# Optimization experiments

Measured on AMD Instinct MI355X. Metric: run time of the kernel, lower is better.

Reference implementation:

```python
import jax, jax.numpy as jnp
import numpy as np
from jax import lax


def _conv(x, w, b, padding):
    # x: NCHW, w: OIHW
    y = lax.conv_general_dilated(x, w, (1, 1), padding,
                                 dimension_numbers=('NCHW', 'OIHW', 'NCHW'))
    return y + b[None, :, None, None]


def setup_inputs() -> dict:
    key = jax.random.key(0)
    ks = jax.random.split(key, 24)
    B = 64
    d = {
        'p2': jax.random.normal(ks[0], (B, 128, 64, 128), jnp.float32),
        'p3': jax.random.normal(ks[1], (B, 128, 32, 64), jnp.float32),
        'p4': jax.random.normal(ks[2], (B, 128, 16, 32), jnp.float32),
        'p5': jax.random.normal(ks[3], (B, 512, 8, 16), jnp.float32),
    }
    def w(k, shape, fan_in):
        return jax.random.normal(k, shape, jnp.float32) * (1.0 / np.sqrt(fan_in))
    # smooth convs 3x3, 128->128
    for i, name in enumerate(['s1', 's2', 's3']):
        d['w_' + name] = w(ks[4 + 2 * i], (128, 128, 3, 3), 128 * 9)
        d['b_' + name] = jnp.zeros((128,), jnp.float32)
    # tidy convs 1x1
    tidy_cin = [128, 128, 128, 512]
    for i in range(4):
        d['w_t%d' % (i + 1)] = w(ks[10 + i], (1, tidy_cin[i], 1, 1), tidy_cin[i])
        d['b_t%d' % (i + 1)] = jnp.zeros((1,), jnp.float32)
    # pl convs (kH,1) on single channel
    pl_kh = [64, 32, 16, 8]
    for i in range(4):
        d['w_pl%d' % (i + 1)] = w(ks[14 + i], (1, 1, pl_kh[i], 1), pl_kh[i])
        d['b_pl%d' % (i + 1)] = jnp.zeros((1,), jnp.float32)
    return d


def reference(p2, p3, p4, p5,
              w_s1, b_s1, w_s2, b_s2, w_s3, b_s3,
              w_t1, b_t1, w_t2, b_t2, w_t3, b_t3, w_t4, b_t4,
              w_pl1, b_pl1, w_pl2, b_pl2, w_pl3, b_pl3, w_pl4, b_pl4):
    B = p2.shape[0]
    # smooth + relu (p5 has no smooth in the original module)
    q2 = jax.nn.relu(_conv(p2, w_s1, b_s1, 'SAME'))
    q3 = jax.nn.relu(_conv(p3, w_s2, b_s2, 'SAME'))
    q4 = jax.nn.relu(_conv(p4, w_s3, b_s3, 'SAME'))
    # tidy 1x1 -> single score channel
    t1 = _conv(q2, w_t1, b_t1, 'VALID')
    t2 = _conv(q3, w_t2, b_t2, 'VALID')
    t3 = _conv(q4, w_t3, b_t3, 'VALID')
    t4 = _conv(p5, w_t4, b_t4, 'VALID')
    # column-pooling convs collapse height to 1 -> per-column scores
    c1 = _conv(t1, w_pl1, b_pl1, 'VALID').reshape(B, -1)  # [B,128]
    c2 = _conv(t2, w_pl2, b_pl2, 'VALID').reshape(B, -1)  # [B,64]
    c3 = _conv(t3, w_pl3, b_pl3, 'VALID').reshape(B, -1)  # [B,32]
    c4 = _conv(t4, w_pl4, b_pl4, 'VALID').reshape(B, -1)  # [B,16]
    return jnp.concatenate([c1, c2, c3, c4], axis=1)      # [B,240]
```

## Files before the change

kernel.cpp:

```cpp
#include <hip/hip_runtime.h>


typedef short s8v __attribute__((ext_vector_type(8)));
typedef float f4v __attribute__((ext_vector_type(4)));

__device__ __forceinline__ unsigned short f32_bf16_rne(float f) {
  union { float f; unsigned int u; } v;
  v.f = f;
  unsigned int u = v.u;
  u += 0x7FFFu + ((u >> 16) & 1u);
  return (unsigned short)(u >> 16);
}

__device__ __forceinline__ void gld_lds16(const unsigned short* g, unsigned short* l) {
  __builtin_amdgcn_global_load_lds(
      (const __attribute__((address_space(1))) unsigned int*)g,
      (__attribute__((address_space(3))) unsigned int*)l, 16, 0, 0);
}

__global__ void prep_x_k(const float* __restrict__ p,
                         unsigned short* __restrict__ out,
                         int H, int W) {
  size_t idx = (size_t)blockIdx.x * 256 + threadIdx.x;
  int HW = H * W;
  int w = (int)(idx % W);
  size_t r = idx / W;
  int h = (int)(r % H); r /= H;
  int qg = (int)(r & 3); r >>= 2;
  int chunk = (int)(r & 3); r >>= 2;
  int b = (int)r;
  const float* src = p + (((size_t)(b * 128 + chunk * 32 + qg * 8)) * H + h) * W + w;
  s8v v;
#pragma unroll
  for (int i = 0; i < 8; ++i) v[i] = (short)f32_bf16_rne(src[(size_t)i * HW]);
  *(s8v*)(out + idx * 8) = v;
}

__global__ void prep_w_k(const float* __restrict__ w1,
                         const float* __restrict__ w2,
                         const float* __restrict__ w3,
                         unsigned short* __restrict__ out) {
  int idx = blockIdx.x * 256 + threadIdx.x;
  if (idx >= 442368) return;
  int i    = idx & 7;
  int cout = (idx >> 3) & 127;
  int t    = idx >> 10;
  int qg = t & 3; t >>= 2;
  int kw = t % 3; t /= 3;
  int kh = t % 3; t /= 3;
  int chunk = t & 3; t >>= 2;
  int s = t;
  const float* w = (s == 0) ? w1 : ((s == 1) ? w2 : w3);
  int cin = chunk * 32 + qg * 8 + i;
  out[idx] = f32_bf16_rne(w[((cout * 128 + cin) * 3 + kh) * 3 + kw]);
}

__global__ void init_out_k(float* __restrict__ out,
                           const float* bt1, const float* bt2,
                           const float* bt3, const float* bt4,
                           const float* wpl1, const float* bpl1,
                           const float* wpl2, const float* bpl2,
                           const float* wpl3, const float* bpl3,
                           const float* wpl4, const float* bpl4) {
  int idx = blockIdx.x * 256 + threadIdx.x;
  if (idx >= 64 * 240) return;
  int c = idx % 240;
  const float* wpl; const float* bpl; const float* bt; int H;
  if (c < 128)      { wpl = wpl1; bpl = bpl1; bt = bt1; H = 64; }
  else if (c < 192) { wpl = wpl2; bpl = bpl2; bt = bt2; H = 32; }
  else if (c < 224) { wpl = wpl3; bpl = bpl3; bt = bt3; H = 16; }
  else              { wpl = wpl4; bpl = bpl4; bt = bt4; H = 8;  }
  float s = 0.f;
  for (int h = 0; h < H; ++h) s += wpl[h];
  out[idx] = bt[0] * s + bpl[0];
}

__global__ void level4_k(const float* __restrict__ p5,
                         const float* __restrict__ w_t4,
                         const float* __restrict__ w_pl4,
                         float* __restrict__ out) {
  int b = blockIdx.x;
  int z = blockIdx.y;
  int t = threadIdx.x;
  int w = t & 15, g = t >> 4;
  const float* base = p5 + (size_t)b * 65536 + z * 16384;
  const float* wt = w_t4 + z * 128;
  float acc = 0.f;
  for (int j = g; j < 1024; j += 16) {
    acc += wt[j >> 3] * w_pl4[j & 7] * base[j * 16 + w];
  }
  acc += __shfl_xor(acc, 16);
  acc += __shfl_xor(acc, 32);
  if ((t & 48) == 0) atomicAdd(&out[b * 240 + 224 + w], acc);
}

template<int H, int W, int R, int COLBASE>
__global__ __launch_bounds__(256, 2)
void conv_level_k(const unsigned short* __restrict__ xp,
                  const unsigned short* __restrict__ wl,
                  const float* __restrict__ b_s,
                  const float* __restrict__ w_t,
                  const float* __restrict__ w_pl,
                  float* __restrict__ out) {
  constexpr int ROWS = R + 2;
  constexpr int WP = W + 2;
  __shared__ __align__(16) unsigned short Xs[4][ROWS][WP][8];
  __shared__ __align__(16) unsigned short Ws[3][4][128][8];

  const int tid = threadIdx.x;
  const int wave = tid >> 6, lane = tid & 63;
  const int lm = lane & 15, q = lane >> 4;
  const int h0 = blockIdx.x * R;
  const int b  = blockIdx.y;

  int rr[4], ww[4], xbase[4];
#pragma unroll
  for (int nt = 0; nt < 4; ++nt) {
    int n = wave * 64 + nt * 16 + lm;
    rr[nt] = n / W;
    ww[nt] = n % W;
    xbase[nt] = ((q * ROWS + rr[nt]) * WP + ww[nt]) * 16;
  }
  const int woff = (q * 128 + lm) * 16;

  f4v acc[8][4];
#pragma unroll
  for (int mt = 0; mt < 8; ++mt)
#pragma unroll
    for (int nt = 0; nt < 4; ++nt)
      acc[mt][nt] = (f4v){0.f, 0.f, 0.f, 0.f};

  const s8v Z8 = {0, 0, 0, 0, 0, 0, 0, 0};
  for (int t = tid; t < 4 * ROWS * 2; t += 256) {
    int qg = t / (ROWS * 2);
    int r2 = t % (ROWS * 2);
    *(s8v*)&Xs[qg][r2 >> 1][(r2 & 1) ? (WP - 1) : 0][0] = Z8;
  }

  const unsigned short* xb = xp + (size_t)b * 16 * H * W * 8;
  unsigned short* WsF = &Ws[0][0][0][0];
  const char* XsB = (const char*)&Xs[0][0][0][0];
  const char* WsB = (const char*)WsF;

  for (int chunk = 0; chunk < 4; ++chunk) {
    __syncthreads();
    {
      const int qg = wave;
      const unsigned short* xq = xb + (size_t)(chunk * 4 + qg) * H * W * 8;
#pragma unroll
      for (int row = 0; row < ROWS; ++row) {
        int h_in = h0 + row - 1;
        bool ok = (h_in >= 0) && (h_in < H);
        const unsigned short* srow = xq + (size_t)h_in * W * 8;
        if constexpr (W >= 64) {
#pragma unroll
          for (int j = 0; j < W / 64; ++j) {
            if (ok) gld_lds16(srow + j * 512 + lane * 8, &Xs[qg][row][1 + j * 64][0]);
            else    *(s8v*)&Xs[qg][row][1 + j * 64 + lane][0] = Z8;
          }
        } else {
          if (lane < W) {
            s8v v = Z8;
            if (ok) v = *(const s8v*)(srow + lane * 8);
            *(s8v*)&Xs[qg][row][1 + lane][0] = v;
          }
        }
      }
    }
    for (int kh = 0; kh < 3; ++kh) {
      if (kh) __syncthreads();
      {
        const unsigned short* wsrc = wl + (size_t)(chunk * 3 + kh) * 12288;
        for (int i2 = wave; i2 < 24; i2 += 4)
          gld_lds16(wsrc + i2 * 512 + lane * 8, WsF + i2 * 512);
      }
      __syncthreads();

      int xk[4];
#pragma unroll
      for (int nt = 0; nt < 4; ++nt) xk[nt] = xbase[nt] + kh * (WP * 16);

#pragma unroll
      for (int kw = 0; kw < 3; ++kw) {
        s8v bf[4];
#pragma unroll
        for (int nt = 0; nt < 4; ++nt)
          bf[nt] = *(const s8v*)(XsB + xk[nt] + kw * 16);
#pragma unroll
        for (int mt = 0; mt < 8; ++mt) {
          s8v af = *(const s8v*)(WsB + kw * 8192 + mt * 256 + woff);
#pragma unroll
          for (int nt = 0; nt < 4; ++nt)
            acc[mt][nt] = __builtin_amdgcn_mfma_f32_16x16x32_bf16(af, bf[nt], acc[mt][nt], 0, 0, 0);
        }
      }
    }
  }

#pragma unroll
  for (int nt = 0; nt < 4; ++nt) {
    float s = 0.f;
#pragma unroll
    for (int mt = 0; mt < 8; ++mt) {
#pragma unroll
      for (int rg = 0; rg < 4; ++rg) {
        int cout = mt * 16 + q * 4 + rg;
        float v = fmaxf(acc[mt][nt][rg] + b_s[cout], 0.f);
        s = fmaf(w_t[cout], v, s);
      }
    }
    s *= w_pl[h0 + rr[nt]];
    s += __shfl_xor(s, 16);
    s += __shfl_xor(s, 32);
    if (lane < 16) atomicAdd(&out[b * 240 + COLBASE + ww[nt]], s);
  }
}

extern "C" void kernel_launch(void* const* d_in, const int* in_sizes, int n_in,
                              void* d_out, int out_size, void* d_ws, size_t ws_size,
                              hipStream_t stream) {
  (void)in_sizes; (void)n_in; (void)out_size; (void)ws_size;
  const float* p2   = (const float*)d_in[0];
  const float* p3   = (const float*)d_in[1];
  const float* p4   = (const float*)d_in[2];
  const float* p5   = (const float*)d_in[3];
  const float* w_s1 = (const float*)d_in[4];
  const float* b_s1 = (const float*)d_in[5];
  const float* w_s2 = (const float*)d_in[6];
  const float* b_s2 = (const float*)d_in[7];
  const float* w_s3 = (const float*)d_in[8];
  const float* b_s3 = (const float*)d_in[9];
  const float* w_t1 = (const float*)d_in[10];
  const float* b_t1 = (const float*)d_in[11];
  const float* w_t2 = (const float*)d_in[12];
  const float* b_t2 = (const float*)d_in[13];
  const float* w_t3 = (const float*)d_in[14];
  const float* b_t3 = (const float*)d_in[15];
  const float* w_t4 = (const float*)d_in[16];
  const float* b_t4 = (const float*)d_in[17];
  const float* w_pl1 = (const float*)d_in[18];
  const float* b_pl1 = (const float*)d_in[19];
  const float* w_pl2 = (const float*)d_in[20];
  const float* b_pl2 = (const float*)d_in[21];
  const float* w_pl3 = (const float*)d_in[22];
  const float* b_pl3 = (const float*)d_in[23];
  const float* w_pl4 = (const float*)d_in[24];
  const float* b_pl4 = (const float*)d_in[25];

  unsigned short* wp  = (unsigned short*)d_ws;
  unsigned short* xp1 = wp + 442368;
  unsigned short* xp2 = xp1 + (size_t)64 * 16 * 64 * 128 * 8;
  unsigned short* xp3 = xp2 + (size_t)64 * 16 * 32 * 64 * 8;
  float* out = (float*)d_out;

  prep_w_k<<<dim3(1728), dim3(256), 0, stream>>>(w_s1, w_s2, w_s3, wp);
  prep_x_k<<<dim3(32768), dim3(256), 0, stream>>>(p2, xp1, 64, 128);
  prep_x_k<<<dim3(8192),  dim3(256), 0, stream>>>(p3, xp2, 32, 64);
  prep_x_k<<<dim3(2048),  dim3(256), 0, stream>>>(p4, xp3, 16, 32);
  init_out_k<<<dim3(60), dim3(256), 0, stream>>>(out, b_t1, b_t2, b_t3, b_t4,
                                                 w_pl1, b_pl1, w_pl2, b_pl2,
                                                 w_pl3, b_pl3, w_pl4, b_pl4);
  conv_level_k<64, 128, 2, 0><<<dim3(32, 64), dim3(256), 0, stream>>>(
      xp1, wp, b_s1, w_t1, w_pl1, out);
  conv_level_k<32, 64, 4, 128><<<dim3(8, 64), dim3(256), 0, stream>>>(
      xp2, wp + 147456, b_s2, w_t2, w_pl2, out);
  conv_level_k<16, 32, 8, 192><<<dim3(2, 64), dim3(256), 0, stream>>>(
      xp3, wp + 294912, b_s3, w_t3, w_pl3, out);
  level4_k<<<dim3(64, 4), dim3(256), 0, stream>>>(p5, w_t4, w_pl4, out);
}
```

Baseline: 701.3 us.

## Fuse fp32-to-bf16 input conversion into conv kernel and register-prefetch weights

Removes the separate prep_x_k passes, which wrote bf16 channel-packed copies of p2/p3/p4 to workspace. The conv kernel now reads the fp32 NCHW input directly, converts to bf16 and packs into LDS, including the zero halo. Weight tiles are prefetched into registers one kh step ahead and stored to LDS between barriers, replacing global_load_lds. This avoids the extra global write and reread of the activations, but each tile load now does strided scalar fp32 reads. Halo rows and columns are also read and converted again by neighbouring blocks.

```diff
diff --git a/kernel.cpp b/kernel.cpp
--- a/kernel.cpp
+++ b/kernel.cpp
@@ -10,30 +10,6 @@
   unsigned int u = v.u;
   u += 0x7FFFu + ((u >> 16) & 1u);
   return (unsigned short)(u >> 16);
-}
-
-__device__ __forceinline__ void gld_lds16(const unsigned short* g, unsigned short* l) {
-  __builtin_amdgcn_global_load_lds(
-      (const __attribute__((address_space(1))) unsigned int*)g,
-      (__attribute__((address_space(3))) unsigned int*)l, 16, 0, 0);
-}
-
-__global__ void prep_x_k(const float* __restrict__ p,
-                         unsigned short* __restrict__ out,
-                         int H, int W) {
-  size_t idx = (size_t)blockIdx.x * 256 + threadIdx.x;
-  int HW = H * W;
-  int w = (int)(idx % W);
-  size_t r = idx / W;
-  int h = (int)(r % H); r /= H;
-  int qg = (int)(r & 3); r >>= 2;
-  int chunk = (int)(r & 3); r >>= 2;
-  int b = (int)r;
-  const float* src = p + (((size_t)(b * 128 + chunk * 32 + qg * 8)) * H + h) * W + w;
-  s8v v;
-#pragma unroll
-  for (int i = 0; i < 8; ++i) v[i] = (short)f32_bf16_rne(src[(size_t)i * HW]);
-  *(s8v*)(out + idx * 8) = v;
 }
 
 __global__ void prep_w_k(const float* __restrict__ w1,
@@ -96,7 +72,7 @@
 
 template<int H, int W, int R, int COLBASE>
 __global__ __launch_bounds__(256, 2)
-void conv_level_k(const unsigned short* __restrict__ xp,
+void conv_level_k(const float* __restrict__ p,
                   const unsigned short* __restrict__ wl,
                   const float* __restrict__ b_s,
                   const float* __restrict__ w_t,
@@ -104,6 +80,8 @@
                   float* __restrict__ out) {
   constexpr int ROWS = R + 2;
   constexpr int WP = W + 2;
+  constexpr int HW = H * W;
+  constexpr int NIT = 4 * ROWS * WP;
   __shared__ __align__(16) unsigned short Xs[4][ROWS][WP][8];
   __shared__ __align__(16) unsigned short Ws[3][4][128][8];
 
@@ -131,50 +109,52 @@
       acc[mt][nt] = (f4v){0.f, 0.f, 0.f, 0.f};
 
   const s8v Z8 = {0, 0, 0, 0, 0, 0, 0, 0};
-  for (int t = tid; t < 4 * ROWS * 2; t += 256) {
-    int qg = t / (ROWS * 2);
-    int r2 = t % (ROWS * 2);
-    *(s8v*)&Xs[qg][r2 >> 1][(r2 & 1) ? (WP - 1) : 0][0] = Z8;
-  }
-
-  const unsigned short* xb = xp + (size_t)b * 16 * H * W * 8;
-  unsigned short* WsF = &Ws[0][0][0][0];
+  const float* pb = p + (size_t)b * 128 * HW;
   const char* XsB = (const char*)&Xs[0][0][0][0];
-  const char* WsB = (const char*)WsF;
+  const char* WsB = (const char*)&Ws[0][0][0][0];
+
+  s8v wreg[6];
+  const unsigned short* wseg = wl + wave * 512 + lane * 8;
+  unsigned short* wdst = &Ws[0][0][0][0] + wave * 512 + lane * 8;
+
+#define LOAD_W(chunk, kh) do {                                        \
+    const unsigned short* _s = wseg + ((chunk) * 3 + (kh)) * 12288;   \
+    _Pragma("unroll")                                                 \
+    for (int s = 0; s < 6; ++s) wreg[s] = *(const s8v*)(_s + s * 2048); \
+  } while (0)
+
+#define STORE_W() do {                                                \
+    _Pragma("unroll")                                                 \
+    for (int s = 0; s < 6; ++s) *(s8v*)(wdst + s * 2048) = wreg[s];   \
+  } while (0)
+
+  LOAD_W(0, 0);
 
   for (int chunk = 0; chunk < 4; ++chunk) {
     __syncthreads();
-    {
-      const int qg = wave;
-      const unsigned short* xq = xb + (size_t)(chunk * 4 + qg) * H * W * 8;
-#pragma unroll
-      for (int row = 0; row < ROWS; ++row) {
-        int h_in = h0 + row - 1;
-        bool ok = (h_in >= 0) && (h_in < H);
-        const unsigned short* srow = xq + (size_t)h_in * W * 8;
-        if constexpr (W >= 64) {
-#pragma unroll
-          for (int j = 0; j < W / 64; ++j) {
-            if (ok) gld_lds16(srow + j * 512 + lane * 8, &Xs[qg][row][1 + j * 64][0]);
-            else    *(s8v*)&Xs[qg][row][1 + j * 64 + lane][0] = Z8;
-          }
-        } else {
-          if (lane < W) {
-            s8v v = Z8;
-            if (ok) v = *(const s8v*)(srow + lane * 8);
-            *(s8v*)&Xs[qg][row][1 + lane][0] = v;
-          }
-        }
-      }
+    for (int it = tid; it < NIT; it += 256) {
+      int pos = it % WP;
+      int rem = it / WP;
+      int row = rem % ROWS;
+      int qg  = rem / ROWS;
+      int h_in = h0 + row - 1;
+      int w_g  = pos - 1;
+      s8v v = Z8;
+      if (h_in >= 0 && h_in < H && w_g >= 0 && w_g < W) {
+        const float* src = pb + (size_t)(chunk * 32 + qg * 8) * HW + h_in * W + w_g;
+#pragma unroll
+        for (int i = 0; i < 8; ++i) v[i] = (short)f32_bf16_rne(src[(size_t)i * HW]);
+      }
+      *(s8v*)&Xs[qg][row][pos][0] = v;
     }
+    STORE_W();
+    __syncthreads();
+
+#pragma unroll
     for (int kh = 0; kh < 3; ++kh) {
-      if (kh) __syncthreads();
-      {
-        const unsigned short* wsrc = wl + (size_t)(chunk * 3 + kh) * 12288;
-        for (int i2 = wave; i2 < 24; i2 += 4)
-          gld_lds16(wsrc + i2 * 512 + lane * 8, WsF + i2 * 512);
-      }
-      __syncthreads();
+      int nc = (kh == 2) ? ((chunk < 3) ? chunk + 1 : 3) : chunk;
+      int nk = (kh == 2) ? 0 : kh + 1;
+      LOAD_W(nc, nk);
 
       int xk[4];
 #pragma unroll
@@ -194,8 +174,15 @@
             acc[mt][nt] = __builtin_amdgcn_mfma_f32_16x16x32_bf16(af, bf[nt], acc[mt][nt], 0, 0, 0);
         }
       }
+      if (kh < 2) {
+        __syncthreads();
+        STORE_W();
+        __syncthreads();
+      }
     }
   }
+#undef LOAD_W
+#undef STORE_W
 
 #pragma unroll
   for (int nt = 0; nt < 4; ++nt) {
@@ -247,24 +234,18 @@
   const float* w_pl4 = (const float*)d_in[24];
   const float* b_pl4 = (const float*)d_in[25];
 
-  unsigned short* wp  = (unsigned short*)d_ws;
-  unsigned short* xp1 = wp + 442368;
-  unsigned short* xp2 = xp1 + (size_t)64 * 16 * 64 * 128 * 8;
-  unsigned short* xp3 = xp2 + (size_t)64 * 16 * 32 * 64 * 8;
+  unsigned short* wp = (unsigned short*)d_ws;
   float* out = (float*)d_out;
 
   prep_w_k<<<dim3(1728), dim3(256), 0, stream>>>(w_s1, w_s2, w_s3, wp);
-  prep_x_k<<<dim3(32768), dim3(256), 0, stream>>>(p2, xp1, 64, 128);
-  prep_x_k<<<dim3(8192),  dim3(256), 0, stream>>>(p3, xp2, 32, 64);
-  prep_x_k<<<dim3(2048),  dim3(256), 0, stream>>>(p4, xp3, 16, 32);
   init_out_k<<<dim3(60), dim3(256), 0, stream>>>(out, b_t1, b_t2, b_t3, b_t4,
                                                  w_pl1, b_pl1, w_pl2, b_pl2,
                                                  w_pl3, b_pl3, w_pl4, b_pl4);
   conv_level_k<64, 128, 2, 0><<<dim3(32, 64), dim3(256), 0, stream>>>(
-      xp1, wp, b_s1, w_t1, w_pl1, out);
+      p2, wp, b_s1, w_t1, w_pl1, out);
   conv_level_k<32, 64, 4, 128><<<dim3(8, 64), dim3(256), 0, stream>>>(
-      xp2, wp + 147456, b_s2, w_t2, w_pl2, out);
+      p3, wp + 147456, b_s2, w_t2, w_pl2, out);
   conv_level_k<16, 32, 8, 192><<<dim3(2, 64), dim3(256), 0, stream>>>(
-      xp3, wp + 294912, b_s3, w_t3, w_pl3, out);
+      p4, wp + 294912, b_s3, w_t3, w_pl3, out);
   level4_k<<<dim3(64, 4), dim3(256), 0, stream>>>(p5, w_t4, w_pl4, out);
 }
```

New measurement: 680.1 us. 3.0% less time.
